# Kernel optimization log

Measured on AMD Instinct MI355X. Metric: run time of the kernel, lower is better.

The kernel has to match this reference:

```python
import jax, jax.numpy as jnp
import numpy as np

WINDOW_LENGTH = 512
ORDER = 26


def hann_window(n):
    # periodic Hann (matches torch.hann_window default)
    i = jnp.arange(n, dtype=jnp.float32)
    return 0.5 * (1.0 - jnp.cos(2.0 * jnp.pi * i / n))


def upsample_linear(g, hop):
    # F.interpolate(mode='linear', align_corners=False), scale_factor=hop
    B, F = g.shape
    j = jnp.arange(F * hop, dtype=jnp.float32)
    src = jnp.clip((j + 0.5) / hop - 0.5, 0.0, F - 1.0)
    i0 = jnp.floor(src).astype(jnp.int32)
    i1 = jnp.minimum(i0 + 1, F - 1)
    w = src - i0.astype(jnp.float32)
    return g[:, i0] * (1.0 - w) + g[:, i1] * w


def lpc_synthesis_batch(x, a):
    # all-pole IIR: y[n] = x[n] - sum_k a[k] * y[n-1-k]; x [N,W], a [N,order]
    N, W = x.shape
    order = a.shape[1]

    def step(carry, xt):  # carry [N,order] newest-first, xt [N]
        yt = xt - jnp.sum(a * carry, axis=1)
        carry = jnp.concatenate([yt[:, None], carry[:, :-1]], axis=1)
        return carry, yt

    _, y = jax.lax.scan(step, jnp.zeros((N, order), x.dtype), x.T)
    return y.T  # [N, W]


def setup_inputs() -> dict:
    key = jax.random.key(0)
    k1, k2, k3 = jax.random.split(key, 3)
    B, T, F = 32, 128000, 1000
    ex = jax.random.normal(k1, (B, T), dtype=jnp.float32)
    gain = jax.random.uniform(k2, (B, F), dtype=jnp.float32)
    # small coefficients keep the all-pole filter stable
    a = jax.random.normal(k3, (B, F, ORDER), dtype=jnp.float32) * 0.05
    window = hann_window(WINDOW_LENGTH)
    return {"ex": ex, "gain": gain, "a": a, "window": window, "hop_length": 128}


def reference(ex, gain, a, window, hop_length):
    W = window.shape[0]
    pad = (W - hop_length) // 2
    B = ex.shape[0]
    ug = upsample_linear(gain, hop_length)  # [B, F*hop]
    T = min(ex.shape[1], ug.shape[1])
    exg = ex[:, :T] * ug[:, :T]
    exp = jnp.pad(exg, ((0, 0), (pad, pad)))
    nframes = (exp.shape[1] - W) // hop_length + 1
    idx = jnp.arange(nframes)[:, None] * hop_length + jnp.arange(W)[None, :]  # [F,W]
    unfolded = exp[:, idx]  # [B, F, W]
    a_ = a[:, :nframes].reshape(-1, a.shape[-1])
    filt = lpc_synthesis_batch(unfolded.reshape(-1, W), a_).reshape(B, nframes, W)
    windowed = filt * window  # window applied per in-frame sample (diag kernel)
    L = (nframes - 1) * hop_length + W
    flat_idx = idx.reshape(-1)
    ola = jnp.zeros((B, L), filt.dtype).at[:, flat_idx].add(windowed.reshape(B, -1))
    norm = jnp.zeros((L,), filt.dtype).at[flat_idx].add(jnp.tile(window, nframes))
    return ola[:, pad:L - pad] / norm[pad:L - pad]
```

## Files before the change

kernel.cpp:

```cpp
#include <hip/hip_runtime.h>
#include <hip/hip_bf16.h>

#define BATCH   32
#define TLEN    128000
#define FGAIN   1000
#define ORDER   26
#define WLEN    512
#define HOP     128
#define PAD     192
#define TPAD    (TLEN + 2*PAD)
#define NFRAME  1000
#define NTOT    (BATCH*NFRAME)

#define CHUNK   64
#define NCHUNK  ((NFRAME + CHUNK - 1) / CHUNK)
#define XS_SPAN (CHUNK*HOP + WLEN - HOP)
#define XS_LDS  8656

__global__ __launch_bounds__(256) void k_exg(const float* __restrict__ ex,
                                             const float* __restrict__ gain,
                                             float* __restrict__ exg) {
  int gid = blockIdx.x * 256 + threadIdx.x;
  const int total4 = BATCH * TPAD / 4;
  if (gid >= total4) return;
  int idx = gid * 4;
  int b  = idx / TPAD;
  int r0 = idx - b * TPAD;
  const float* __restrict__ gr  = gain + b * FGAIN;
  const float* __restrict__ exr = ex + (size_t)b * TLEN;
  float v[4];
#pragma unroll
  for (int c = 0; c < 4; ++c) {
    int j = r0 + c - PAD;
    float val = 0.0f;
    if (j >= 0 && j < TLEN) {
      float src = ((float)j + 0.5f) * (1.0f / (float)HOP) - 0.5f;
      src = fminf(fmaxf(src, 0.0f), (float)(FGAIN - 1));
      int   i0 = (int)src;
      float w  = src - (float)i0;
      int   i1 = (i0 < FGAIN - 1) ? i0 + 1 : FGAIN - 1;
      float g  = gr[i0] * (1.0f - w) + gr[i1] * w;
      val = exr[j] * g;
    }
    v[c] = val;
  }
  float4 o = make_float4(v[0], v[1], v[2], v[3]);
  *reinterpret_cast<float4*>(exg + idx) = o;
}

__global__ __launch_bounds__(64) void k_lpc(const float* __restrict__ exg,
                                            const float* __restrict__ acoef,
                                            float* __restrict__ fw) {
  __shared__ float xs[XS_LDS];

  const int lane = threadIdx.x;
  const int n0   = blockIdx.x * CHUNK;
  const int b    = blockIdx.y;
  const float* __restrict__ xrow = exg + (size_t)b * TPAD;

  for (int i = lane; i < XS_SPAN / 4; i += 64) {
    int s = 4 * i;
    int g = n0 * HOP + s;
    float4 v = make_float4(0.f, 0.f, 0.f, 0.f);
    if (g < TPAD)
      v = *reinterpret_cast<const float4*>(xrow + g);
    int base = s + (s >> 7);
    xs[base + 0] = v.x;  xs[base + 1] = v.y;
    xs[base + 2] = v.z;  xs[base + 3] = v.w;
  }
  __syncthreads();

  const bool valid = (n0 + lane) < NFRAME;
  int f = b * NFRAME + n0 + lane;
  int f_cl = f < NTOT ? f : NTOT - 1;
  const float* __restrict__ ap = acoef + (size_t)f_cl * ORDER;
  float* __restrict__ op = fw + (size_t)f * WLEN;

  float a[ORDER], h[ORDER];
#pragma unroll
  for (int q = 0; q < 13; ++q) {
    float2 v = *reinterpret_cast<const float2*>(ap + 2 * q);
    a[2 * q] = v.x;  a[2 * q + 1] = v.y;
  }
#pragma unroll
  for (int k = 0; k < ORDER; ++k) h[k] = 0.0f;

  float buf[52];

#define LPC_STEP(s) {                                                      \
    float xv = buf[(s)];                                                   \
    float p0 = xv, p1 = 0.f, p2 = 0.f, p3 = 0.f;                           \
    _Pragma("unroll")                                                      \
    for (int k = 1; k < ORDER; ++k) {                                      \
      float hv = h[((s) - 1 - k + 2 * ORDER) % ORDER];                     \
      int sel = k & 3;                                                     \
      if      (sel == 0) p0 -= a[k] * hv;                                  \
      else if (sel == 1) p1 -= a[k] * hv;                                  \
      else if (sel == 2) p2 -= a[k] * hv;                                  \
      else               p3 -= a[k] * hv;                                  \
    }                                                                      \
    float rest = (p0 + p1) + (p2 + p3);                                    \
    float y = rest - a[0] * h[((s) + ORDER - 1) % ORDER];                  \
    h[(s) % ORDER] = y;                                                    \
    buf[(s)] = y;                                                          \
  }

#define LOAD_BUF(nq) {                                                     \
    _Pragma("unroll")                                                      \
    for (int q = 0; q < (nq); ++q) {                                       \
      int u = t + 4 * q;                                                   \
      int base = lane * 129 + u + (u >> 7);                                \
      buf[4 * q + 0] = xs[base + 0];                                       \
      buf[4 * q + 1] = xs[base + 1];                                       \
      buf[4 * q + 2] = xs[base + 2];                                       \
      buf[4 * q + 3] = xs[base + 3];                                       \
    }                                                                      \
  }

  int t = 0;
  for (int sb = 0; sb < 9; ++sb) {
    LOAD_BUF(13)
#pragma unroll
    for (int s = 0; s < 52; ++s) {
      LPC_STEP(s)
    }
    if (valid) {
#pragma unroll
      for (int q = 0; q < 13; ++q) {
        float4 v = make_float4(buf[4 * q + 0], buf[4 * q + 1],
                               buf[4 * q + 2], buf[4 * q + 3]);
        *reinterpret_cast<float4*>(op + t + 4 * q) = v;
      }
    }
    t += 52;
  }
  LOAD_BUF(11)
#pragma unroll
  for (int s = 0; s < 44; ++s) {
    LPC_STEP(s)
  }
  if (valid) {
#pragma unroll
    for (int q = 0; q < 11; ++q) {
      float4 v = make_float4(buf[4 * q + 0], buf[4 * q + 1],
                             buf[4 * q + 2], buf[4 * q + 3]);
      *reinterpret_cast<float4*>(op + t + 4 * q) = v;
    }
  }
#undef LPC_STEP
#undef LOAD_BUF
}

__global__ __launch_bounds__(256) void k_ola(const float* __restrict__ fw,
                                             const float* __restrict__ win,
                                             float* __restrict__ out) {
  int gid = blockIdx.x * 256 + threadIdx.x;
  const int total4 = BATCH * TLEN / 4;
  if (gid >= total4) return;
  int idx = gid * 4;
  int b  = idx / TLEN;
  int j0 = idx - b * TLEN;
  int p0 = j0 + PAD;

  int lo = (p0 - 381) / HOP;
  if (lo < 0) lo = 0;
  int hi = p0 / HOP;
  if (hi > NFRAME - 1) hi = NFRAME - 1;

  float ax = 0.f, ay = 0.f, az = 0.f, aw = 0.f;
  float nx = 0.f, ny = 0.f, nz = 0.f, nw = 0.f;
  for (int n = lo; n <= hi; ++n) {
    int w0 = p0 - n * HOP;
    const float4 fv = *reinterpret_cast<const float4*>(fw + ((size_t)b * NFRAME + n) * WLEN + w0);
    const float4 wv = *reinterpret_cast<const float4*>(win + w0);
    ax += fv.x * wv.x;  ay += fv.y * wv.y;  az += fv.z * wv.z;  aw += fv.w * wv.w;
    nx += wv.x;         ny += wv.y;         nz += wv.z;         nw += wv.w;
  }
  float4 o = make_float4(ax / nx, ay / ny, az / nz, aw / nw);
  *reinterpret_cast<float4*>(out + idx) = o;
}

extern "C" void kernel_launch(void* const* d_in, const int* in_sizes, int n_in,
                              void* d_out, int out_size, void* d_ws, size_t ws_size,
                              hipStream_t stream) {
  const float* ex   = (const float*)d_in[0];
  const float* gain = (const float*)d_in[1];
  const float* a    = (const float*)d_in[2];
  const float* win  = (const float*)d_in[3];
  float* outp = (float*)d_out;

  float* exg = (float*)d_ws;
  float* fw  = exg + (size_t)BATCH * TPAD;

  {
    int total4 = BATCH * TPAD / 4;
    int blocks = (total4 + 255) / 256;
    hipLaunchKernelGGL(k_exg, dim3(blocks), dim3(256), 0, stream, ex, gain, exg);
  }
  {
    hipLaunchKernelGGL(k_lpc, dim3(NCHUNK, BATCH), dim3(64), 0, stream, exg, a, fw);
  }
  {
    int total4 = BATCH * TLEN / 4;
    int blocks = (total4 + 255) / 256;
    hipLaunchKernelGGL(k_ola, dim3(blocks), dim3(256), 0, stream, fw, win, outp);
  }
}
```

Measured before the change: 131.1 us.

## Fuse gain upsampling into LPC kernel and coalesce frame output stores via LDS

Removes the separate excitation-times-gain kernel and its workspace round trip. Each LPC block now loads the needed gain values into shared memory and computes the gained excitation while staging it. Filter outputs are also written to a padded shared buffer and stored cooperatively, so global writes are coalesced across frames instead of each lane writing its own strided row. This adds block barriers and shared-memory traffic in the inner recurrence, and the extra LDS use may lower occupancy.

Result: no change. 132.2 us (+0.8%).

```diff
diff --git a/kernel.cpp b/kernel.cpp
--- a/kernel.cpp
+++ b/kernel.cpp
@@ -16,65 +16,59 @@
 #define NCHUNK  ((NFRAME + CHUNK - 1) / CHUNK)
 #define XS_SPAN (CHUNK*HOP + WLEN - HOP)
 #define XS_LDS  8656
-
-__global__ __launch_bounds__(256) void k_exg(const float* __restrict__ ex,
-                                             const float* __restrict__ gain,
-                                             float* __restrict__ exg) {
-  int gid = blockIdx.x * 256 + threadIdx.x;
-  const int total4 = BATCH * TPAD / 4;
-  if (gid >= total4) return;
-  int idx = gid * 4;
-  int b  = idx / TPAD;
-  int r0 = idx - b * TPAD;
-  const float* __restrict__ gr  = gain + b * FGAIN;
-  const float* __restrict__ exr = ex + (size_t)b * TLEN;
-  float v[4];
-#pragma unroll
-  for (int c = 0; c < 4; ++c) {
-    int j = r0 + c - PAD;
-    float val = 0.0f;
-    if (j >= 0 && j < TLEN) {
-      float src = ((float)j + 0.5f) * (1.0f / (float)HOP) - 0.5f;
-      src = fminf(fmaxf(src, 0.0f), (float)(FGAIN - 1));
-      int   i0 = (int)src;
-      float w  = src - (float)i0;
-      int   i1 = (i0 < FGAIN - 1) ? i0 + 1 : FGAIN - 1;
-      float g  = gr[i0] * (1.0f - w) + gr[i1] * w;
-      val = exr[j] * g;
-    }
-    v[c] = val;
-  }
-  float4 o = make_float4(v[0], v[1], v[2], v[3]);
-  *reinterpret_cast<float4*>(exg + idx) = o;
-}
-
-__global__ __launch_bounds__(64) void k_lpc(const float* __restrict__ exg,
+#define GS_LDS  80
+#define YSTRIDE 53
+
+__global__ __launch_bounds__(64) void k_lpc(const float* __restrict__ ex,
+                                            const float* __restrict__ gain,
                                             const float* __restrict__ acoef,
                                             float* __restrict__ fw) {
   __shared__ float xs[XS_LDS];
+  __shared__ float gs[GS_LDS];
+  __shared__ float ys[CHUNK * YSTRIDE];
 
   const int lane = threadIdx.x;
   const int n0   = blockIdx.x * CHUNK;
   const int b    = blockIdx.y;
-  const float* __restrict__ xrow = exg + (size_t)b * TPAD;
+  const float* __restrict__ exr = ex + (size_t)b * TLEN;
+  const float* __restrict__ gr  = gain + b * FGAIN;
+
+  const int GBASE = n0 - 2;
+  for (int i = lane; i < 72; i += 64) {
+    int gidx = GBASE + i;
+    gidx = gidx < 0 ? 0 : (gidx > FGAIN - 1 ? FGAIN - 1 : gidx);
+    gs[i] = gr[gidx];
+  }
+  __syncthreads();
 
   for (int i = lane; i < XS_SPAN / 4; i += 64) {
     int s = 4 * i;
-    int g = n0 * HOP + s;
-    float4 v = make_float4(0.f, 0.f, 0.f, 0.f);
-    if (g < TPAD)
-      v = *reinterpret_cast<const float4*>(xrow + g);
+    int j = n0 * HOP + s - PAD;
+    float vv[4] = {0.f, 0.f, 0.f, 0.f};
+    if (j >= 0 && j < TLEN) {
+      float4 e = *reinterpret_cast<const float4*>(exr + j);
+      float ee[4] = {e.x, e.y, e.z, e.w};
+#pragma unroll
+      for (int c = 0; c < 4; ++c) {
+        float src = ((float)(j + c) + 0.5f) * (1.0f / (float)HOP) - 0.5f;
+        src = fminf(fmaxf(src, 0.0f), (float)(FGAIN - 1));
+        int   i0 = (int)src;
+        float w  = src - (float)i0;
+        int   i1 = i0 + 1; if (i1 > FGAIN - 1) i1 = FGAIN - 1;
+        float g  = gs[i0 - GBASE] * (1.0f - w) + gs[i1 - GBASE] * w;
+        vv[c] = ee[c] * g;
+      }
+    }
     int base = s + (s >> 7);
-    xs[base + 0] = v.x;  xs[base + 1] = v.y;
-    xs[base + 2] = v.z;  xs[base + 3] = v.w;
+    xs[base + 0] = vv[0];  xs[base + 1] = vv[1];
+    xs[base + 2] = vv[2];  xs[base + 3] = vv[3];
   }
   __syncthreads();
 
-  const bool valid = (n0 + lane) < NFRAME;
   int f = b * NFRAME + n0 + lane;
   int f_cl = f < NTOT ? f : NTOT - 1;
   const float* __restrict__ ap = acoef + (size_t)f_cl * ORDER;
-  float* __restrict__ op = fw + (size_t)f * WLEN;
+  const size_t fwrow0 = (size_t)(b * NFRAME + n0) * WLEN;
 
   float a[ORDER], h[ORDER];
 #pragma unroll
@@ -102,7 +96,7 @@
     float rest = (p0 + p1) + (p2 + p3);                                    \
     float y = rest - a[0] * h[((s) + ORDER - 1) % ORDER];                  \
     h[(s) % ORDER] = y;                                                    \
-    buf[(s)] = y;                                                          \
+    ys[lane * YSTRIDE + (s)] = y;                                          \
   }
 
 #define LOAD_BUF(nq) {                                                     \
@@ -117,6 +111,29 @@
     }                                                                      \
   }
 
+#define STORE_YS(nq) {                                                     \
+    __syncthreads();                                                       \
+    _Pragma("unroll")                                                      \
+    for (int jj = 0; jj < 4; ++jj) {                                       \
+      int q = (lane & 3) + 4 * jj;                                         \
+      if (q < (nq)) {                                                      \
+        _Pragma("unroll")                                                  \
+        for (int rr = 0; rr < 4; ++rr) {                                   \
+          int r = rr * 16 + (lane >> 2);                                   \
+          if ((n0 + r) < NFRAME) {                                         \
+            float4 vv = make_float4(ys[r * YSTRIDE + 4 * q + 0],           \
+                                    ys[r * YSTRIDE + 4 * q + 1],           \
+                                    ys[r * YSTRIDE + 4 * q + 2],           \
+                                    ys[r * YSTRIDE + 4 * q + 3]);          \
+            *reinterpret_cast<float4*>(fw + fwrow0 + (size_t)r * WLEN      \
+                                       + t + 4 * q) = vv;                  \
+          }                                                                \
+        }                                                                  \
+      }                                                                    \
+    }                                                                      \
+    __syncthreads();                                                       \
+  }
+
   int t = 0;
   for (int sb = 0; sb < 9; ++sb) {
     LOAD_BUF(13)
@@ -124,14 +141,7 @@
     for (int s = 0; s < 52; ++s) {
       LPC_STEP(s)
     }
-    if (valid) {
-#pragma unroll
-      for (int q = 0; q < 13; ++q) {
-        float4 v = make_float4(buf[4 * q + 0], buf[4 * q + 1],
-                               buf[4 * q + 2], buf[4 * q + 3]);
-        *reinterpret_cast<float4*>(op + t + 4 * q) = v;
-      }
-    }
+    STORE_YS(13)
     t += 52;
   }
   LOAD_BUF(11)
@@ -139,16 +149,10 @@
   for (int s = 0; s < 44; ++s) {
     LPC_STEP(s)
   }
-  if (valid) {
-#pragma unroll
-    for (int q = 0; q < 11; ++q) {
-      float4 v = make_float4(buf[4 * q + 0], buf[4 * q + 1],
-                             buf[4 * q + 2], buf[4 * q + 3]);
-      *reinterpret_cast<float4*>(op + t + 4 * q) = v;
-    }
-  }
+  STORE_YS(11)
 #undef LPC_STEP
 #undef LOAD_BUF
+#undef STORE_YS
 }
 
 __global__ __launch_bounds__(256) void k_ola(const float* __restrict__ fw,
@@ -189,16 +193,11 @@
   const float* win  = (const float*)d_in[3];
   float* outp = (float*)d_out;
 
-  float* exg = (float*)d_ws;
-  float* fw  = exg + (size_t)BATCH * TPAD;
+  float* fw = (float*)d_ws;
 
   {
-    int total4 = BATCH * TPAD / 4;
-    int blocks = (total4 + 255) / 256;
-    hipLaunchKernelGGL(k_exg, dim3(blocks), dim3(256), 0, stream, ex, gain, exg);
-  }
-  {
-    hipLaunchKernelGGL(k_lpc, dim3(NCHUNK, BATCH), dim3(64), 0, stream, exg, a, fw);
+    hipLaunchKernelGGL(k_lpc, dim3(NCHUNK, BATCH), dim3(64), 0, stream,
+                       ex, gain, a, fw);
   }
   {
     int total4 = BATCH * TLEN / 4;
```
